# Kernel optimization log

Measured on AMD Instinct MI355X. Metric: run time of the kernel, lower is better.

The kernel has to match this reference:

```python
import jax, jax.numpy as jnp
import numpy as np

# 4-neighbor cross stencil deltas from CONNECTION_FLAGS_3x3_small
DELTAS = ((-1, 0), (0, -1), (0, 1), (1, 0))


def setup_inputs() -> dict:
    key = jax.random.key(0)
    k1, k2, k3 = jax.random.split(key, 3)
    B, G, C, H, W = 4, 8, 32, 128, 128
    patchs = jax.random.normal(k1, (B, G, C, H, W), dtype=jnp.float32)
    edge_weights = jax.random.uniform(k2, (B, G, 4, H, W), dtype=jnp.float32)
    node_degree = jax.random.uniform(k3, (B, G, H, W), dtype=jnp.float32)
    return {"patchs": patchs, "edge_weights": edge_weights, "node_degree": node_degree}


def _gather_neighbors(x):
    # x: [B, GC, H, W] -> [B, GC, 4, H, W] with replicate padding (torch 'replicate' == jnp 'edge')
    B, GC, H, W = x.shape
    xp = jnp.pad(x, ((0, 0), (0, 0), (1, 1), (1, 1)), mode='edge')
    nbrs = [xp[:, :, 1 + dh:1 + dh + H, 1 + dw:1 + dw + W] for dh, dw in DELTAS]
    return jnp.stack(nbrs, axis=2)


def reference(patchs, edge_weights, node_degree):
    # patchs: [B, G, C, H, W]; edge_weights: [B, G, 4, H, W]; node_degree unused in forward
    B, G, C, H, W = patchs.shape
    x = patchs.reshape(B, G * C, H, W)
    nbrs = _gather_neighbors(x).reshape(B, G, C, 4, H, W)
    Wx = jnp.einsum('bgcehw,bgehw->bgchw', nbrs, edge_weights)
    return patchs - Wx
```

## Files before the change

kernel.cpp:

```cpp
#include <hip/hip_runtime.h>


#define GLR_H   128
#define GLR_W   128
#define GLR_HW  (GLR_H * GLR_W)

__global__ __launch_bounds__(256) void glr_fwd_kernel(
    const float* __restrict__ patchs,
    const float* __restrict__ ew,
    float* __restrict__ out)
{
    const int tid   = blockIdx.x * 256 + threadIdx.x;
    const int w4    = tid & 31;
    const int h     = (tid >> 5) & 127;
    const int plane = tid >> 12;
    const int bg    = plane >> 5;

    const int w   = w4 << 2;
    const int off = (h << 7) + w;

    const float* __restrict__ P = patchs + (size_t)plane * GLR_HW;
    const float* __restrict__ E = ew + (size_t)bg * 4 * GLR_HW;

    const float4 c4 = *(const float4*)(P + off);
    const int hu = (h == 0)   ? 0   : h - 1;
    const int hd = (h == 127) ? 127 : h + 1;
    const float4 up4 = *(const float4*)(P + (hu << 7) + w);
    const float4 dn4 = *(const float4*)(P + (hd << 7) + w);

    const float lf = (w4 == 0)  ? c4.x : P[off - 1];
    const float rg = (w4 == 31) ? c4.w : P[off + 4];

    const float4 e0 = *(const float4*)(E + off);
    const float4 e1 = *(const float4*)(E + GLR_HW + off);
    const float4 e2 = *(const float4*)(E + 2 * GLR_HW + off);
    const float4 e3 = *(const float4*)(E + 3 * GLR_HW + off);

    float4 o;
    o.x = c4.x - (up4.x * e0.x + lf   * e1.x + c4.y * e2.x + dn4.x * e3.x);
    o.y = c4.y - (up4.y * e0.y + c4.x * e1.y + c4.z * e2.y + dn4.y * e3.y);
    o.z = c4.z - (up4.z * e0.z + c4.y * e1.z + c4.w * e2.z + dn4.z * e3.z);
    o.w = c4.w - (up4.w * e0.w + c4.z * e1.w + rg   * e2.w + dn4.w * e3.w);

    *(float4*)(out + (size_t)plane * GLR_HW + off) = o;
}

extern "C" void kernel_launch(void* const* d_in, const int* in_sizes, int n_in,
                              void* d_out, int out_size, void* d_ws, size_t ws_size,
                              hipStream_t stream) {
    const float* patchs = (const float*)d_in[0];
    const float* ew     = (const float*)d_in[1];
    float* out = (float*)d_out;

    glr_fwd_kernel<<<16384, 256, 0, stream>>>(patchs, ew, out);
}
```

Measured before the change: 137.5 us.

## Reuse edge weights across 8 channels per thread and shuffle horizontal neighbors

```diff
diff --git a/kernel.cpp b/kernel.cpp
--- a/kernel.cpp
+++ b/kernel.cpp
@@ -1,48 +1,62 @@
 #include <hip/hip_runtime.h>
 
 
-#define GLR_H   128
-#define GLR_W   128
-#define GLR_HW  (GLR_H * GLR_W)
+#define GLR_HW 16384
 
 __global__ __launch_bounds__(256) void glr_fwd_kernel(
     const float* __restrict__ patchs,
     const float* __restrict__ ew,
     float* __restrict__ out)
 {
-    const int tid   = blockIdx.x * 256 + threadIdx.x;
-    const int w4    = tid & 31;
-    const int h     = (tid >> 5) & 127;
-    const int plane = tid >> 12;
-    const int bg    = plane >> 5;
+    const int t    = threadIdx.x;
+    const int w4   = t & 31;
+    const int cg   = (t >> 5) & 3;
+    const int hsub = t >> 7;
 
-    const int w   = w4 << 2;
-    const int off = (h << 7) + w;
+    const int bg = blockIdx.x >> 6;
+    const int h  = ((blockIdx.x & 63) << 1) + hsub;
 
-    const float* __restrict__ P = patchs + (size_t)plane * GLR_HW;
-    const float* __restrict__ E = ew + (size_t)bg * 4 * GLR_HW;
+    const int w    = w4 << 2;
+    const int off  = (h << 7) + w;
+    const int hu   = (h == 0)   ? h : h - 1;
+    const int hd   = (h == 127) ? h : h + 1;
+    const int offu = (hu << 7) + w;
+    const int offd = (hd << 7) + w;
 
-    const float4 c4 = *(const float4*)(P + off);
-    const int hu = (h == 0)   ? 0   : h - 1;
-    const int hd = (h == 127) ? 127 : h + 1;
-    const float4 up4 = *(const float4*)(P + (hu << 7) + w);
-    const float4 dn4 = *(const float4*)(P + (hd << 7) + w);
+    const float* __restrict__ E = ew + (size_t)bg * 4 * GLR_HW + off;
+    const float4 e0 = *(const float4*)(E);
+    const float4 e1 = *(const float4*)(E + GLR_HW);
+    const float4 e2 = *(const float4*)(E + 2 * GLR_HW);
+    const float4 e3 = *(const float4*)(E + 3 * GLR_HW);
 
-    const float lf = (w4 == 0)  ? c4.x : P[off - 1];
-    const float rg = (w4 == 31) ? c4.w : P[off + 4];
+    const bool atL = (w4 == 0);
+    const bool atR = (w4 == 31);
 
-    const float4 e0 = *(const float4*)(E + off);
-    const float4 e1 = *(const float4*)(E + GLR_HW + off);
-    const float4 e2 = *(const float4*)(E + 2 * GLR_HW + off);
-    const float4 e3 = *(const float4*)(E + 3 * GLR_HW + off);
+    const size_t planeBase = ((size_t)bg * 32 + (size_t)cg * 8) * GLR_HW;
+    const float* __restrict__ P = patchs + planeBase;
+    float*       __restrict__ O = out    + planeBase;
 
-    float4 o;
-    o.x = c4.x - (up4.x * e0.x + lf   * e1.x + c4.y * e2.x + dn4.x * e3.x);
-    o.y = c4.y - (up4.y * e0.y + c4.x * e1.y + c4.z * e2.y + dn4.y * e3.y);
-    o.z = c4.z - (up4.z * e0.z + c4.y * e1.z + c4.w * e2.z + dn4.z * e3.z);
-    o.w = c4.w - (up4.w * e0.w + c4.z * e1.w + rg   * e2.w + dn4.w * e3.w);
+    #pragma unroll 4
+    for (int c = 0; c < 8; ++c) {
+        const float4 c4  = *(const float4*)(P + off);
+        const float4 up4 = *(const float4*)(P + offu);
+        const float4 dn4 = *(const float4*)(P + offd);
 
-    *(float4*)(out + (size_t)plane * GLR_HW + off) = o;
+        float lf = __shfl_up(c4.w, 1);
+        float rg = __shfl_down(c4.x, 1);
+        if (atL) lf = c4.x;
+        if (atR) rg = c4.w;
+
+        float4 o;
+        o.x = c4.x - (up4.x * e0.x + lf   * e1.x + c4.y * e2.x + dn4.x * e3.x);
+        o.y = c4.y - (up4.y * e0.y + c4.x * e1.y + c4.z * e2.y + dn4.y * e3.y);
+        o.z = c4.z - (up4.z * e0.z + c4.y * e1.z + c4.w * e2.z + dn4.z * e3.z);
+        o.w = c4.w - (up4.w * e0.w + c4.z * e1.w + rg   * e2.w + dn4.w * e3.w);
+
+        *(float4*)(O + off) = o;
+        P += GLR_HW;
+        O += GLR_HW;
+    }
 }
 
 extern "C" void kernel_launch(void* const* d_in, const int* in_sizes, int n_in,
@@ -52,5 +66,5 @@
     const float* ew     = (const float*)d_in[1];
     float* out = (float*)d_out;
 
-    glr_fwd_kernel<<<16384, 256, 0, stream>>>(patchs, ew, out);
+    glr_fwd_kernel<<<2048, 256, 0, stream>>>(patchs, ew, out);
 }
```

Result: faster. 130.9 us (-4.8%).

## Stream eight rows per thread with register sliding window and lane shuffles

Applied to the files above, without the earlier changes.

```diff
diff --git a/kernel.cpp b/kernel.cpp
--- a/kernel.cpp
+++ b/kernel.cpp
@@ -1,48 +1,66 @@
 #include <hip/hip_runtime.h>
 
 
-#define GLR_H   128
-#define GLR_W   128
-#define GLR_HW  (GLR_H * GLR_W)
+#define GLR_HW 16384
 
-__global__ __launch_bounds__(256) void glr_fwd_kernel(
+__global__ __launch_bounds__(256, 8) void glr_fwd_kernel(
     const float* __restrict__ patchs,
     const float* __restrict__ ew,
     float* __restrict__ out)
 {
-    const int tid   = blockIdx.x * 256 + threadIdx.x;
-    const int w4    = tid & 31;
-    const int h     = (tid >> 5) & 127;
-    const int plane = tid >> 12;
-    const int bg    = plane >> 5;
+    const int t  = threadIdx.x;
+    const int w4 = t & 31;
+    const int cl = t >> 5;
 
-    const int w   = w4 << 2;
-    const int off = (h << 7) + w;
+    const int bg     = blockIdx.x >> 6;
+    const int strip  = (blockIdx.x >> 2) & 15;
+    const int cgroup = blockIdx.x & 3;
 
-    const float* __restrict__ P = patchs + (size_t)plane * GLR_HW;
-    const float* __restrict__ E = ew + (size_t)bg * 4 * GLR_HW;
+    const int c     = (cgroup << 3) + cl;
+    const int plane = (bg << 5) + c;
+    const int r0    = strip << 3;
+    const int w     = w4 << 2;
 
-    const float4 c4 = *(const float4*)(P + off);
-    const int hu = (h == 0)   ? 0   : h - 1;
-    const int hd = (h == 127) ? 127 : h + 1;
-    const float4 up4 = *(const float4*)(P + (hu << 7) + w);
-    const float4 dn4 = *(const float4*)(P + (hd << 7) + w);
+    const float* __restrict__ P = patchs + (size_t)plane * GLR_HW + w;
+    float*       __restrict__ O = out    + (size_t)plane * GLR_HW + w;
+    const float* __restrict__ E = ew + (size_t)bg * 4 * GLR_HW + w;
 
-    const float lf = (w4 == 0)  ? c4.x : P[off - 1];
-    const float rg = (w4 == 31) ? c4.w : P[off + 4];
+    const bool atL = (w4 == 0);
+    const bool atR = (w4 == 31);
 
-    const float4 e0 = *(const float4*)(E + off);
-    const float4 e1 = *(const float4*)(E + GLR_HW + off);
-    const float4 e2 = *(const float4*)(E + 2 * GLR_HW + off);
-    const float4 e3 = *(const float4*)(E + 3 * GLR_HW + off);
+    const int rup = (r0 == 0) ? 0 : r0 - 1;
+    float4 up  = *(const float4*)(P + (rup << 7));
+    float4 cur = *(const float4*)(P + (r0 << 7));
+    float4 dn  = *(const float4*)(P + ((r0 + 1) << 7));
 
-    float4 o;
-    o.x = c4.x - (up4.x * e0.x + lf   * e1.x + c4.y * e2.x + dn4.x * e3.x);
-    o.y = c4.y - (up4.y * e0.y + c4.x * e1.y + c4.z * e2.y + dn4.y * e3.y);
-    o.z = c4.z - (up4.z * e0.z + c4.y * e1.z + c4.w * e2.z + dn4.z * e3.z);
-    o.w = c4.w - (up4.w * e0.w + c4.z * e1.w + rg   * e2.w + dn4.w * e3.w);
+    #pragma unroll
+    for (int i = 0; i < 8; ++i) {
+        const int r   = r0 + i;
+        const int ro  = r << 7;
+        const int rn2 = (r + 2 > 127) ? 127 : r + 2;
 
-    *(float4*)(out + (size_t)plane * GLR_HW + off) = o;
+        const float4 dn2 = *(const float4*)(P + (rn2 << 7));
+
+        const float4 e0 = *(const float4*)(E + ro);
+        const float4 e1 = *(const float4*)(E + GLR_HW + ro);
+        const float4 e2 = *(const float4*)(E + 2 * GLR_HW + ro);
+        const float4 e3 = *(const float4*)(E + 3 * GLR_HW + ro);
+
+        float lf = __shfl_up(cur.w, 1);
+        float rg = __shfl_down(cur.x, 1);
+        if (atL) lf = cur.x;
+        if (atR) rg = cur.w;
+
+        float4 o;
+        o.x = cur.x - (up.x * e0.x + lf    * e1.x + cur.y * e2.x + dn.x * e3.x);
+        o.y = cur.y - (up.y * e0.y + cur.x * e1.y + cur.z * e2.y + dn.y * e3.y);
+        o.z = cur.z - (up.z * e0.z + cur.y * e1.z + cur.w * e2.z + dn.z * e3.z);
+        o.w = cur.w - (up.w * e0.w + cur.z * e1.w + rg    * e2.w + dn.w * e3.w);
+
+        *(float4*)(O + ro) = o;
+
+        up = cur; cur = dn; dn = dn2;
+    }
 }
 
 extern "C" void kernel_launch(void* const* d_in, const int* in_sizes, int n_in,
@@ -52,5 +70,5 @@
     const float* ew     = (const float*)d_in[1];
     float* out = (float*)d_out;
 
-    glr_fwd_kernel<<<16384, 256, 0, stream>>>(patchs, ew, out);
+    glr_fwd_kernel<<<2048, 256, 0, stream>>>(patchs, ew, out);
 }
```

Result: faster. 125.8 us (-8.5%).
